# Performance work log

Hardware: AMD Instinct MI355X
Metric: run time of the kernel (lower is better)

## Reference

```python
import jax, jax.numpy as jnp
import numpy as np

N_NODES = 100000
N_EDGES = 1600000
D_FEAT = 64  # node feature dim; apply_func indim = 2*D_FEAT, outdim = D_FEAT


def setup_inputs() -> dict:
    key = jax.random.key(0)
    k1, k2, k3, k4 = jax.random.split(key, 4)
    h = jax.random.normal(k1, (N_NODES, D_FEAT), dtype=jnp.float32)
    src = jax.random.randint(k2, (N_EDGES,), 0, N_NODES, dtype=jnp.int32)
    dst = jax.random.randint(k3, (N_EDGES,), 0, N_NODES, dtype=jnp.int32)
    W = jax.random.normal(k4, (D_FEAT, 2 * D_FEAT), dtype=jnp.float32) / jnp.sqrt(2.0 * D_FEAT)
    b = jnp.zeros((D_FEAT,), dtype=jnp.float32)
    return {"h": h, "W": W, "b": b, "src": src, "dst": dst}


def reference(h, W, b, src, dst):
    n = h.shape[0]
    # message passing: gather source features, mean-reduce per destination node
    msgs = h[src]                                                # [E, D]
    summed = jax.ops.segment_sum(msgs, dst, num_segments=n)     # [N, D]
    deg = jax.ops.segment_sum(jnp.ones(dst.shape, h.dtype), dst, num_segments=n)  # [N]
    c = summed / jnp.maximum(deg, 1.0)[:, None]                 # mean aggregate
    # update: concat(h, c) -> linear -> L2 normalize -> relu
    bundle = jnp.concatenate([h, c], axis=1) @ W.T + b           # [N, D]
    norm = jnp.linalg.norm(bundle, axis=1, keepdims=True)
    bundle = bundle / jnp.maximum(norm, 1e-12)                   # F.normalize(p=2, dim=1)
    new_h = jax.nn.relu(bundle)
    # DGL update_all only touches nodes that received messages
    h_upd = jnp.where(deg[:, None] > 0, new_h, h)
    # residual (indim == outdim)
    return h + h_upd
```

## Files before the change

kernel.cpp:

```cpp
#include <hip/hip_runtime.h>

#define DF 64
#define ELLK 32
#define NB 256
#define BSTR 7168
#define NPB 400
#define NSL 4

typedef __attribute__((ext_vector_type(8))) short bf16x8;
typedef __attribute__((ext_vector_type(4))) float f32x4;

__device__ __forceinline__ unsigned short bf16rne(float f) {
    unsigned u = __float_as_uint(f);
    unsigned r = u + 0x7fffu + ((u >> 16) & 1u);
    return (unsigned short)(r >> 16);
}
__device__ __forceinline__ float b2f(unsigned short u) {
    return __uint_as_float((unsigned)u << 16);
}

__global__ __launch_bounds__(256) void conv_zero(
    const float* __restrict__ h, unsigned short* __restrict__ hbs,
    int* __restrict__ gcur, int* __restrict__ ovfcnt, int N)
{
    int tid = blockIdx.x * 256 + threadIdx.x;
    if (tid < NB) gcur[tid] = 0;
    if (tid == NB) *ovfcnt = 0;
    if (tid < NSL) {
        unsigned short* zp = &hbs[((size_t)tid * (N + 1) + N) * 16];
        ushort4 z = {0, 0, 0, 0};
        *(ushort4*)zp = z; *(ushort4*)(zp + 4) = z;
        *(ushort4*)(zp + 8) = z; *(ushort4*)(zp + 12) = z;
    }
    if (tid < N * 8) {
        int n = tid >> 3, s8 = tid & 7;
        const float* hp = &h[(size_t)n * DF + s8 * 8];
        float4 v0 = *(const float4*)hp;
        float4 v1 = *(const float4*)(hp + 4);
        ushort4 o0, o1;
        o0.x = bf16rne(v0.x); o0.y = bf16rne(v0.y); o0.z = bf16rne(v0.z); o0.w = bf16rne(v0.w);
        o1.x = bf16rne(v1.x); o1.y = bf16rne(v1.y); o1.z = bf16rne(v1.z); o1.w = bf16rne(v1.w);
        unsigned short* op = &hbs[((size_t)(s8 >> 1) * (N + 1) + n) * 16 + (s8 & 1) * 8];
        *(ushort4*)op = o0;
        *(ushort4*)(op + 4) = o1;
    }
}

#define EPT 13
__global__ __launch_bounds__(256) void bin_edges(
    const int* __restrict__ src, const int* __restrict__ dst,
    int* __restrict__ gcur, unsigned* __restrict__ pairs,
    int* __restrict__ ovf, int* __restrict__ ovfcnt, int ovfcap, int E, int N)
{
    __shared__ unsigned hist[NB];
    __shared__ unsigned base_s[NB];
    int t = threadIdx.x;
    for (int i = t; i < NB; i += 256) hist[i] = 0;
    __syncthreads();

    int e0 = blockIdx.x * (EPT * 256);
    unsigned pk[EPT];
    #pragma unroll
    for (int k = 0; k < EPT; ++k) {
        int e = e0 + k * 256 + t;
        pk[k] = 0xFFFFFFFFu;
        if (e < E) {
            int d = dst[e];
            unsigned bkt = (unsigned)(((unsigned long long)d * NB) / (unsigned)N);
            unsigned r = atomicAdd(&hist[bkt], 1u);
            pk[k] = (r << 8) | bkt;
        }
    }
    __syncthreads();
    for (int i = t; i < NB; i += 256)
        base_s[i] = (unsigned)atomicAdd(&gcur[i], (int)hist[i]);
    __syncthreads();

    #pragma unroll
    for (int k = 0; k < EPT; ++k) {
        if (pk[k] != 0xFFFFFFFFu) {
            int e = e0 + k * 256 + t;
            int d = dst[e], s = src[e];
            unsigned bkt = pk[k] & 255u;
            unsigned pos = base_s[bkt] + (pk[k] >> 8);
            if (pos < BSTR) {
                int lo = (int)(((long long)bkt * N + NB - 1) / NB);
                pairs[(size_t)bkt * BSTR + pos] = ((unsigned)(d - lo) << 17) | (unsigned)s;
            } else {
                int p = atomicAdd(ovfcnt, 1);
                if (p < ovfcap) { ovf[2 * p] = d; ovf[2 * p + 1] = s; }
            }
        }
    }
}

__global__ __launch_bounds__(256) void build_ell(
    const unsigned* __restrict__ pairs, const int* __restrict__ gcur,
    int* __restrict__ cnt, int* __restrict__ ell,
    int* __restrict__ ovf, int* __restrict__ ovfcnt, int ovfcap, int N)
{
    __shared__ int ell_l[NPB * ELLK];
    __shared__ int cnt_l[NPB];
    int b = blockIdx.x, t = threadIdx.x;
    int lo = (int)(((long long)b * N + NB - 1) / NB);
    int hi = (int)(((long long)(b + 1) * N + NB - 1) / NB);
    if (hi > N) hi = N;
    int nn = hi - lo;
    for (int i = t; i < nn; i += 256) cnt_l[i] = 0;
    __syncthreads();

    int count = gcur[b]; if (count > BSTR) count = BSTR;
    const unsigned* pb = &pairs[(size_t)b * BSTR];
    for (int i = t; i < count; i += 256) {
        unsigned p = pb[i];
        int ld = (int)(p >> 17);
        int s  = (int)(p & 131071u);
        int slot = atomicAdd(&cnt_l[ld], 1);
        if (slot < ELLK) {
            ell_l[ld * ELLK + (((slot & 7) << 2) | (slot >> 3))] = s;
        } else {
            int q = atomicAdd(ovfcnt, 1);
            if (q < ovfcap) { ovf[2 * q] = lo + ld; ovf[2 * q + 1] = s; }
        }
    }
    __syncthreads();

    int total = nn * ELLK;
    int* eout = &ell[(size_t)lo * ELLK];
    for (int i = t; i < total; i += 256) eout[i] = ell_l[i];
    for (int i = t; i < nn; i += 256) {
        int c = cnt_l[i];
        cnt[lo + i] = c < ELLK ? c : ELLK;
    }
}

__global__ __launch_bounds__(512) void gather_slice(
    const unsigned short* __restrict__ hbs, const int* __restrict__ cnt,
    const int* __restrict__ ell, unsigned short* __restrict__ csum, int N)
{
    int slice = blockIdx.x & 3;
    int wave = threadIdx.x >> 6, lane = threadIdx.x & 63;
    const int ns = lane >> 4;
    const int q  = lane & 15;
    const int nb = q >> 1;
    const int fp = q & 1;
    const unsigned short* tab = hbs + (size_t)slice * (N + 1) * 16;
    unsigned short* cs = csum + (size_t)slice * N * 16;

    int gw = (blockIdx.x >> 2) * 8 + wave;
    int nw = (gridDim.x >> 2) * 8;

    for (int n0 = gw * 4; n0 < N; n0 += nw * 4) {
        int n = n0 + ns;
        bool valid = (n < N);
        int m = valid ? cnt[n] : 0;
        const int* erow = &ell[(size_t)(valid ? n : 0) * ELLK];
        int4 pv = *(const int4*)(erow + nb * 4);
        int id0 = (nb      < m) ? pv.x : N;
        int id1 = (nb +  8 < m) ? pv.y : N;
        int id2 = (nb + 16 < m) ? pv.z : N;
        int id3 = (nb + 24 < m) ? pv.w : N;

        bf16x8 v0 = *(const bf16x8*)&tab[(size_t)id0 * 16 + fp * 8];
        bf16x8 v1 = *(const bf16x8*)&tab[(size_t)id1 * 16 + fp * 8];
        bf16x8 v2 = *(const bf16x8*)&tab[(size_t)id2 * 16 + fp * 8];
        bf16x8 v3 = *(const bf16x8*)&tab[(size_t)id3 * 16 + fp * 8];

        f32x4 lo, hi;
        #pragma unroll
        for (int i = 0; i < 4; ++i) {
            lo[i] = (b2f((unsigned short)v0[i])     + b2f((unsigned short)v1[i]))
                  + (b2f((unsigned short)v2[i])     + b2f((unsigned short)v3[i]));
            hi[i] = (b2f((unsigned short)v0[4 + i]) + b2f((unsigned short)v1[4 + i]))
                  + (b2f((unsigned short)v2[4 + i]) + b2f((unsigned short)v3[4 + i]));
        }

        #pragma unroll
        for (int msk = 2; msk <= 8; msk <<= 1) {
            #pragma unroll
            for (int i = 0; i < 4; ++i) {
                lo[i] += __shfl_xor(lo[i], msk);
                hi[i] += __shfl_xor(hi[i], msk);
            }
        }

        if (valid && nb == 0) {
            bf16x8 o;
            o[0] = (short)bf16rne(lo[0]); o[1] = (short)bf16rne(lo[1]);
            o[2] = (short)bf16rne(lo[2]); o[3] = (short)bf16rne(lo[3]);
            o[4] = (short)bf16rne(hi[0]); o[5] = (short)bf16rne(hi[1]);
            o[6] = (short)bf16rne(hi[2]); o[7] = (short)bf16rne(hi[3]);
            *(bf16x8*)&cs[(size_t)n * 16 + fp * 8] = o;
        }
    }
}

__global__ __launch_bounds__(256) void sage_update_mfma(
    const float* __restrict__ h, const float* __restrict__ W,
    const float* __restrict__ b, const int* __restrict__ cnt,
    const unsigned short* __restrict__ hbs,
    const unsigned short* __restrict__ csum,
    const int* __restrict__ ovf, const int* __restrict__ ovfcnt,
    int ovfcap, float* __restrict__ out, int N)
{
    const int lane = threadIdx.x & 63;
    const int wave = threadIdx.x >> 6;
    const int c = lane & 15;
    const int q = lane >> 4;

    bf16x8 bf[4][4];
    #pragma unroll
    for (int nt = 0; nt < 4; ++nt) {
        #pragma unroll
        for (int kt = 0; kt < 4; ++kt) {
            const float* wp = &W[(size_t)(nt * 16 + c) * 128 + kt * 32 + q * 8];
            float4 w0 = *(const float4*)wp;
            float4 w1 = *(const float4*)(wp + 4);
            bf16x8 f;
            f[0] = (short)bf16rne(w0.x); f[1] = (short)bf16rne(w0.y);
            f[2] = (short)bf16rne(w0.z); f[3] = (short)bf16rne(w0.w);
            f[4] = (short)bf16rne(w1.x); f[5] = (short)bf16rne(w1.y);
            f[6] = (short)bf16rne(w1.z); f[7] = (short)bf16rne(w1.w);
            bf[nt][kt] = f;
        }
    }
    float bias[4];
    #pragma unroll
    for (int nt = 0; nt < 4; ++nt) bias[nt] = b[nt * 16 + c];

    int oc = *ovfcnt; if (oc > ovfcap) oc = ovfcap;

    int gwave = blockIdx.x * 4 + wave;
    int nwave = gridDim.x * 4;
    int ntiles = (N + 15) >> 4;
    const int sl0 = q >> 1;
    const int hf  = (q & 1) * 8;

    for (int tile = gwave; tile < ntiles; tile += nwave) {
        int n0 = tile << 4;
        int nm = n0 + c;
        int nmc = nm < N ? nm : N - 1;
        int deg = cnt[nmc];
        int extra = 0;
        if (oc > 0) {
            for (int t = 0; t < oc; ++t)
                if (ovf[2 * t] == nm) extra++;
        }
        int dtot = deg + extra;
        float inv = 1.0f / fmaxf((float)dtot, 1.0f);

        bf16x8 a0 = *(const bf16x8*)&hbs[((size_t)sl0 * (N + 1) + nmc) * 16 + hf];
        bf16x8 a1 = *(const bf16x8*)&hbs[((size_t)(sl0 + 2) * (N + 1) + nmc) * 16 + hf];
        bf16x8 a2, a3;
        #pragma unroll
        for (int kc = 0; kc < 2; ++kc) {
            int sl = kc * 2 + sl0;
            bf16x8 u = *(const bf16x8*)&csum[((size_t)sl * N + nmc) * 16 + hf];
            float e[8];
            #pragma unroll
            for (int i = 0; i < 8; ++i) e[i] = b2f((unsigned short)u[i]);
            if (oc > 0) {
                for (int t = 0; t < oc; ++t) {
                    if (ovf[2 * t] == nm) {
                        bf16x8 hu = *(const bf16x8*)&hbs[((size_t)sl * (N + 1) + ovf[2 * t + 1]) * 16 + hf];
                        #pragma unroll
                        for (int i = 0; i < 8; ++i) e[i] += b2f((unsigned short)hu[i]);
                    }
                }
            }
            bf16x8 f;
            #pragma unroll
            for (int i = 0; i < 8; ++i) f[i] = (short)bf16rne(e[i] * inv);
            if (kc == 0) a2 = f; else a3 = f;
        }

        f32x4 acc0 = {bias[0], bias[0], bias[0], bias[0]};
        f32x4 acc1 = {bias[1], bias[1], bias[1], bias[1]};
        f32x4 acc2 = {bias[2], bias[2], bias[2], bias[2]};
        f32x4 acc3 = {bias[3], bias[3], bias[3], bias[3]};
        acc0 = __builtin_amdgcn_mfma_f32_16x16x32_bf16(a0, bf[0][0], acc0, 0, 0, 0);
        acc0 = __builtin_amdgcn_mfma_f32_16x16x32_bf16(a1, bf[0][1], acc0, 0, 0, 0);
        acc0 = __builtin_amdgcn_mfma_f32_16x16x32_bf16(a2, bf[0][2], acc0, 0, 0, 0);
        acc0 = __builtin_amdgcn_mfma_f32_16x16x32_bf16(a3, bf[0][3], acc0, 0, 0, 0);
        acc1 = __builtin_amdgcn_mfma_f32_16x16x32_bf16(a0, bf[1][0], acc1, 0, 0, 0);
        acc1 = __builtin_amdgcn_mfma_f32_16x16x32_bf16(a1, bf[1][1], acc1, 0, 0, 0);
        acc1 = __builtin_amdgcn_mfma_f32_16x16x32_bf16(a2, bf[1][2], acc1, 0, 0, 0);
        acc1 = __builtin_amdgcn_mfma_f32_16x16x32_bf16(a3, bf[1][3], acc1, 0, 0, 0);
        acc2 = __builtin_amdgcn_mfma_f32_16x16x32_bf16(a0, bf[2][0], acc2, 0, 0, 0);
        acc2 = __builtin_amdgcn_mfma_f32_16x16x32_bf16(a1, bf[2][1], acc2, 0, 0, 0);
        acc2 = __builtin_amdgcn_mfma_f32_16x16x32_bf16(a2, bf[2][2], acc2, 0, 0, 0);
        acc2 = __builtin_amdgcn_mfma_f32_16x16x32_bf16(a3, bf[2][3], acc2, 0, 0, 0);
        acc3 = __builtin_amdgcn_mfma_f32_16x16x32_bf16(a0, bf[3][0], acc3, 0, 0, 0);
        acc3 = __builtin_amdgcn_mfma_f32_16x16x32_bf16(a1, bf[3][1], acc3, 0, 0, 0);
        acc3 = __builtin_amdgcn_mfma_f32_16x16x32_bf16(a2, bf[3][2], acc3, 0, 0, 0);
        acc3 = __builtin_amdgcn_mfma_f32_16x16x32_bf16(a3, bf[3][3], acc3, 0, 0, 0);

        float ss[4];
        #pragma unroll
        for (int r = 0; r < 4; ++r)
            ss[r] = acc0[r] * acc0[r] + acc1[r] * acc1[r]
                  + acc2[r] * acc2[r] + acc3[r] * acc3[r];
        #pragma unroll
        for (int msk = 1; msk <= 8; msk <<= 1) {
            ss[0] += __shfl_xor(ss[0], msk);
            ss[1] += __shfl_xor(ss[1], msk);
            ss[2] += __shfl_xor(ss[2], msk);
            ss[3] += __shfl_xor(ss[3], msk);
        }
        #pragma unroll
        for (int r = 0; r < 4; ++r) {
            int nr = n0 + q * 4 + r;
            int dr = __shfl(deg + extra, q * 4 + r);
            if (nr < N) {
                float rin = 1.0f / fmaxf(sqrtf(ss[r]), 1e-12f);
                const float* hp = &h[(size_t)nr * DF + c];
                float hv0 = hp[0], hv1 = hp[16], hv2 = hp[32], hv3 = hp[48];
                bool up = dr > 0;
                float o0 = hv0 + (up ? fmaxf(acc0[r] * rin, 0.f) : hv0);
                float o1 = hv1 + (up ? fmaxf(acc1[r] * rin, 0.f) : hv1);
                float o2 = hv2 + (up ? fmaxf(acc2[r] * rin, 0.f) : hv2);
                float o3 = hv3 + (up ? fmaxf(acc3[r] * rin, 0.f) : hv3);
                float* op = &out[(size_t)nr * DF + c];
                op[0] = o0; op[16] = o1; op[32] = o2; op[48] = o3;
            }
        }
    }
}

extern "C" void kernel_launch(void* const* d_in, const int* in_sizes, int n_in,
                              void* d_out, int out_size, void* d_ws, size_t ws_size,
                              hipStream_t stream) {
    const float* h   = (const float*)d_in[0];
    const float* W   = (const float*)d_in[1];
    const float* b   = (const float*)d_in[2];
    const int*   src = (const int*)d_in[3];
    const int*   dst = (const int*)d_in[4];
    float* out = (float*)d_out;

    const int N = in_sizes[0] / DF;
    const int E = in_sizes[3];

    int* cnt    = (int*)d_ws;
    int* ovfcnt = cnt + N;
    int* gcur   = cnt + ((N + 31) & ~15);
    int* ell    = gcur + ((NB + 15) & ~15);
    unsigned short* hbs  = (unsigned short*)(ell + (((size_t)N * ELLK + 15) & ~(size_t)15));
    unsigned short* csum = hbs + (((size_t)(N + 1) * DF + 15) & ~(size_t)15);
    unsigned* pairs = (unsigned*)(csum + (((size_t)N * DF + 15) & ~(size_t)15));
    int* ovf    = (int*)(pairs + (size_t)NB * BSTR);
    size_t used = (size_t)((char*)ovf - (char*)d_ws);
    int ovfcap  = (ws_size > used + 64) ? (int)((ws_size - used) / 8 - 4) : 0;

    conv_zero<<<(N * 8 + 255) / 256, 256, 0, stream>>>(h, hbs, gcur, ovfcnt, N);

    bin_edges<<<(E + EPT * 256 - 1) / (EPT * 256), 256, 0, stream>>>(
        src, dst, gcur, pairs, ovf, ovfcnt, ovfcap, E, N);

    build_ell<<<NB, 256, 0, stream>>>(pairs, gcur, cnt, ell, ovf, ovfcnt, ovfcap, N);

    gather_slice<<<2048, 512, 0, stream>>>(hbs, cnt, ell, csum, N);

    sage_update_mfma<<<512, 256, 0, stream>>>(
        h, W, b, cnt, hbs, csum, ovf, ovfcnt, ovfcap, out, N);
}
```

Baseline: 200.3 us.

## Double bucket count, rotate global atomics, predicate ELL gathers instead of zero row

Raises the number of destination buckets to 512, which halves the per-bucket stride and the nodes per ELL-build block so more blocks can work in parallel with less shared memory each. The per-block global atomics that reserve bucket space are now issued in a rotated order per block and skipped for empty buckets, to spread contention on the counters. In the gather kernel, padded slots are skipped with predicated loads instead of reading a zeroed dummy row, so the dummy row setup is removed and fewer loads are issued for low-degree nodes. Smaller buckets raise the chance of overflow into the slower overflow path, and the predicated loads add divergence.

```diff
diff --git a/kernel.cpp b/kernel.cpp
--- a/kernel.cpp
+++ b/kernel.cpp
@@ -2,9 +2,9 @@
 
 #define DF 64
 #define ELLK 32
-#define NB 256
-#define BSTR 7168
-#define NPB 400
+#define NB 512
+#define BSTR 3584
+#define NPB 196
 #define NSL 4
 
 typedef __attribute__((ext_vector_type(8))) short bf16x8;
@@ -26,12 +26,6 @@
     int tid = blockIdx.x * 256 + threadIdx.x;
     if (tid < NB) gcur[tid] = 0;
     if (tid == NB) *ovfcnt = 0;
-    if (tid < NSL) {
-        unsigned short* zp = &hbs[((size_t)tid * (N + 1) + N) * 16];
-        ushort4 z = {0, 0, 0, 0};
-        *(ushort4*)zp = z; *(ushort4*)(zp + 4) = z;
-        *(ushort4*)(zp + 8) = z; *(ushort4*)(zp + 12) = z;
-    }
     if (tid < N * 8) {
         int n = tid >> 3, s8 = tid & 7;
         const float* hp = &h[(size_t)n * DF + s8 * 8];
@@ -68,12 +62,16 @@
             int d = dst[e];
             unsigned bkt = (unsigned)(((unsigned long long)d * NB) / (unsigned)N);
             unsigned r = atomicAdd(&hist[bkt], 1u);
-            pk[k] = (r << 8) | bkt;
-        }
-    }
-    __syncthreads();
-    for (int i = t; i < NB; i += 256)
-        base_s[i] = (unsigned)atomicAdd(&gcur[i], (int)hist[i]);
+            pk[k] = (r << 9) | bkt;
+        }
+    }
+    __syncthreads();
+    int rot = (blockIdx.x * 67) & (NB - 1);
+    for (int i = t; i < NB; i += 256) {
+        int ii = (i + rot) & (NB - 1);
+        unsigned hv = hist[ii];
+        if (hv) base_s[ii] = (unsigned)atomicAdd(&gcur[ii], (int)hv);
+    }
     __syncthreads();
 
     #pragma unroll
@@ -81,8 +79,8 @@
         if (pk[k] != 0xFFFFFFFFu) {
             int e = e0 + k * 256 + t;
             int d = dst[e], s = src[e];
-            unsigned bkt = pk[k] & 255u;
-            unsigned pos = base_s[bkt] + (pk[k] >> 8);
+            unsigned bkt = pk[k] & (NB - 1u);
+            unsigned pos = base_s[bkt] + (pk[k] >> 9);
             if (pos < BSTR) {
                 int lo = (int)(((long long)bkt * N + NB - 1) / NB);
                 pairs[(size_t)bkt * BSTR + pos] = ((unsigned)(d - lo) << 17) | (unsigned)s;
@@ -156,15 +154,15 @@
         int m = valid ? cnt[n] : 0;
         const int* erow = &ell[(size_t)(valid ? n : 0) * ELLK];
         int4 pv = *(const int4*)(erow + nb * 4);
-        int id0 = (nb      < m) ? pv.x : N;
-        int id1 = (nb +  8 < m) ? pv.y : N;
-        int id2 = (nb + 16 < m) ? pv.z : N;
-        int id3 = (nb + 24 < m) ? pv.w : N;
-
-        bf16x8 v0 = *(const bf16x8*)&tab[(size_t)id0 * 16 + fp * 8];
-        bf16x8 v1 = *(const bf16x8*)&tab[(size_t)id1 * 16 + fp * 8];
-        bf16x8 v2 = *(const bf16x8*)&tab[(size_t)id2 * 16 + fp * 8];
-        bf16x8 v3 = *(const bf16x8*)&tab[(size_t)id3 * 16 + fp * 8];
+
+        bf16x8 v0 = {0,0,0,0,0,0,0,0};
+        bf16x8 v1 = {0,0,0,0,0,0,0,0};
+        bf16x8 v2 = {0,0,0,0,0,0,0,0};
+        bf16x8 v3 = {0,0,0,0,0,0,0,0};
+        if (nb      < m) v0 = *(const bf16x8*)&tab[(size_t)pv.x * 16 + fp * 8];
+        if (nb +  8 < m) v1 = *(const bf16x8*)&tab[(size_t)pv.y * 16 + fp * 8];
+        if (nb + 16 < m) v2 = *(const bf16x8*)&tab[(size_t)pv.z * 16 + fp * 8];
+        if (nb + 24 < m) v3 = *(const bf16x8*)&tab[(size_t)pv.w * 16 + fp * 8];
 
         f32x4 lo, hi;
         #pragma unroll
```

Measured after the change: 202.8 us. About the same (+1.2%).
